# Kernel optimization log

Hardware: AMD Instinct MI355X
Metric: run time of the kernel (lower is better)

## Reference

```python
import jax, jax.numpy as jnp
import numpy as np

B, T, E, D, N, L, NF = 4, 2048, 512, 512, 16, 4, 2048


def setup_inputs() -> dict:
    key = jax.random.key(0)
    ks = jax.random.split(key, 12)
    r = lambda k, s, sc=1.0: jax.random.normal(k, s, dtype=jnp.float32) * sc
    return {
        "text_emb": r(ks[0], (B, T, E)),
        "W_in": r(ks[1], (E, D), 1.0 / np.sqrt(E).astype(np.float32)),
        "b_in": jnp.zeros((D,), jnp.float32),
        "freq_pe": r(ks[2], (NF, D), 0.02),
        # diagonal-SSM (S4D) params per layer, stacked on leading L axis
        "A_log": r(ks[3], (L, D, N), 0.5),
        "B_ssm": r(ks[4], (L, D, N), 0.5),
        "C_ssm": r(ks[5], (L, D, N), 0.5),
        "log_dt": r(ks[6], (L, D), 0.5) - 4.6,  # dt ~ 0.01
        "D_skip": r(ks[7], (L, D), 0.5),
        "ln_f0_scale": jnp.ones((D,), jnp.float32),
        "ln_f0_bias": jnp.zeros((D,), jnp.float32),
        "W_f0": r(ks[8], (D, 1), 1.0 / np.sqrt(D).astype(np.float32)),
        "b_f0": jnp.zeros((1,), jnp.float32),
        "ln_en_scale": jnp.ones((D,), jnp.float32),
        "ln_en_bias": jnp.zeros((D,), jnp.float32),
        "W_en": r(ks[9], (D, 1), 1.0 / np.sqrt(D).astype(np.float32)),
        "b_en": jnp.zeros((1,), jnp.float32),
    }


def _layernorm(x, scale, bias, eps=1e-5):
    mu = jnp.mean(x, axis=-1, keepdims=True)
    var = jnp.mean(jnp.square(x - mu), axis=-1, keepdims=True)
    return (x - mu) * jax.lax.rsqrt(var + eps) * scale + bias


def _s4_layer(h, A_log, Bm, Cm, log_dt, Dsk):
    # h: [B, T, D]; diagonal SSM with ZOH discretization, scanned over T.
    dt = jnp.exp(log_dt)                 # [D]
    A = -jnp.exp(A_log)                  # [D, N], stable (negative real)
    Abar = jnp.exp(dt[:, None] * A)      # [D, N]
    Bbar = (Abar - 1.0) / A * Bm         # [D, N]
    u_t = jnp.transpose(h, (1, 0, 2))    # [T, B, D]
    x0 = jnp.zeros((h.shape[0], h.shape[2], A.shape[1]), h.dtype)  # [B, D, N]

    def step(x, u):
        x = Abar * x + Bbar * u[..., None]          # [B, D, N]
        y = jnp.einsum('bdn,dn->bd', x, Cm)         # readout
        return x, y

    _, ys = jax.lax.scan(step, x0, u_t)             # ys: [T, B, D]
    y = jnp.transpose(ys, (1, 0, 2)) + Dsk * h      # D skip connection
    return h + jax.nn.gelu(y)                       # residual + activation


def _forward(text_emb, W_in, b_in, freq_pe, A_log, B_ssm, C_ssm, log_dt,
             D_skip, ln_f0_scale, ln_f0_bias, W_f0, b_f0,
             ln_en_scale, ln_en_bias, W_en, b_en):
    x = text_emb @ W_in + b_in                      # [B, T, D]
    Tlen = x.shape[1]
    nf = freq_pe.shape[0]
    if nf >= Tlen:                                  # static-shape crop
        freq = freq_pe[:Tlen]
    else:                                           # static-shape edge pad
        pad = jnp.repeat(freq_pe[-1:], Tlen - nf, axis=0)
        freq = jnp.concatenate([freq_pe, pad], axis=0)
    h = x + freq[None, :, :]
    for l in range(A_log.shape[0]):
        h = _s4_layer(h, A_log[l], B_ssm[l], C_ssm[l], log_dt[l], D_skip[l])
    f0 = (_layernorm(h, ln_f0_scale, ln_f0_bias) @ W_f0 + b_f0)[..., 0]
    en = (_layernorm(h, ln_en_scale, ln_en_bias) @ W_en + b_en)[..., 0]
    return f0, en


def reference(text_emb, W_in, b_in, freq_pe, A_log, B_ssm, C_ssm, log_dt,
              D_skip, ln_f0_scale, ln_f0_bias, W_f0, b_f0,
              ln_en_scale, ln_en_bias, W_en, b_en):
    return _forward(text_emb, W_in, b_in, freq_pe, A_log, B_ssm, C_ssm,
                    log_dt, D_skip, ln_f0_scale, ln_f0_bias, W_f0, b_f0,
                    ln_en_scale, ln_en_bias, W_en, b_en)
```

## Files before the change

kernel.cpp:

```cpp
#include <hip/hip_runtime.h>

#define B_   4
#define T_   2048
#define E_   512
#define D_   512
#define N_   16
#define L_   4
#define TCH  16

typedef __bf16 bf16x8 __attribute__((ext_vector_type(8)));
typedef float  f32x4  __attribute__((ext_vector_type(4)));
typedef float  f32x2  __attribute__((ext_vector_type(2)));
typedef unsigned short us8 __attribute__((ext_vector_type(8)));

__device__ __forceinline__ float us2f(unsigned short u) {
    return __uint_as_float(((unsigned int)u) << 16);
}
__device__ __forceinline__ unsigned short f2us(float f) {
    unsigned int u = __float_as_uint(f);
    unsigned int r = (u + 0x7fffu + ((u >> 16) & 1u)) >> 16;
    return (unsigned short)r;
}
__device__ __forceinline__ float ldin(const void* p, int i, unsigned int f) {
    return f ? ((const float*)p)[i] : us2f(((const unsigned short*)p)[i]);
}
__device__ __forceinline__ unsigned int probe_f32(const void* lnfs) {
    return (((const unsigned int*)lnfs)[0] == 0x3F800000u) ? 1u : 0u;
}
__device__ __forceinline__ f32x2 pk_fma(f32x2 a, f32x2 b, f32x2 c) {
    f32x2 d;
    asm("v_pk_fma_f32 %0, %1, %2, %3" : "=v"(d) : "v"(a), "v"(b), "v"(c));
    return d;
}
__device__ __forceinline__ f32x2 pk_mul(f32x2 a, f32x2 b) {
    f32x2 d;
    asm("v_pk_mul_f32 %0, %1, %2" : "=v"(d) : "v"(a), "v"(b));
    return d;
}
template<int CTRL, int RM>
__device__ __forceinline__ f32x2 dpp2(f32x2 v) {
    f32x2 r;
    r[0] = __int_as_float(__builtin_amdgcn_update_dpp(0, __float_as_int(v[0]), CTRL, RM, 0xF, true));
    r[1] = __int_as_float(__builtin_amdgcn_update_dpp(0, __float_as_int(v[1]), CTRL, RM, 0xF, true));
    return r;
}

#define PA    0
#define PB    32768
#define PC    65536
#define PDT   98304
#define PDSK  100352
#define PLFS  102400
#define PLFB  102912
#define PWF   103424
#define PLES  103936
#define PLEB  104448
#define PWEN  104960
#define PSC   105472
#define PRM_N 105474

#define NB_TEXT 2048
#define NB_PRM  413
#define NB_WT   64
#define NB_S4P  128

__global__ __launch_bounds__(256) void prep_kernel(
    const void* X, const void* Win,
    const void* A_log, const void* B_ssm, const void* C_ssm,
    const void* log_dt, const void* D_skip,
    const void* lnfs, const void* lnfb, const void* Wf0,
    const void* lnes, const void* lneb, const void* Wen,
    const void* bf0, const void* ben,
    unsigned short* __restrict__ textc, unsigned short* __restrict__ Wt,
    float* __restrict__ P, float* __restrict__ P2, float* __restrict__ P3) {
    __shared__ float tile[64 * 65];
    unsigned int f = probe_f32(lnfs);
    int bid = blockIdx.x;
    if (bid < NB_TEXT) {
        int i = (bid * 256 + threadIdx.x) * 8;
        if (f) {
            const float* xf = (const float*)X;
            us8 r;
#pragma unroll
            for (int j = 0; j < 8; j++) r[j] = f2us(xf[i + j]);
            *(us8*)(textc + i) = r;
        } else {
            *(us8*)(textc + i) = *(const us8*)((const unsigned short*)X + i);
        }
    } else if (bid < NB_TEXT + NB_PRM) {
        int i = (bid - NB_TEXT) * 256 + threadIdx.x;
        if      (i < PB)     P[i] = ldin(A_log,  i - PA,   f);
        else if (i < PC)     P[i] = ldin(B_ssm,  i - PB,   f);
        else if (i < PDT)    P[i] = ldin(C_ssm,  i - PC,   f);
        else if (i < PDSK)   P[i] = ldin(log_dt, i - PDT,  f);
        else if (i < PLFS)   P[i] = ldin(D_skip, i - PDSK, f);
        else if (i < PLFB)   P[i] = ldin(lnfs,   i - PLFS, f);
        else if (i < PWF)    P[i] = ldin(lnfb,   i - PLFB, f);
        else if (i < PLES)   P[i] = ldin(Wf0,    i - PWF,  f);
        else if (i < PLEB)   P[i] = ldin(lnes,   i - PLES, f);
        else if (i < PWEN)   P[i] = ldin(lneb,   i - PLEB, f);
        else if (i < PSC)    P[i] = ldin(Wen,    i - PWEN, f);
        else if (i == PSC)     P[i] = ldin(bf0, 0, f);
        else if (i == PSC + 1) P[i] = ldin(ben, 0, f);
    } else if (bid < NB_TEXT + NB_PRM + NB_WT) {
        int tb = bid - (NB_TEXT + NB_PRM);
        int d0 = (tb >> 3) * 64, e0 = (tb & 7) * 64;
        int r = threadIdx.x >> 6, i = threadIdx.x & 63;
#pragma unroll
        for (int k = 0; k < 16; k++) {
            int e = k * 4 + r;
            tile[e * 65 + i] = ldin(Win, (e0 + e) * D_ + d0 + i, f);
        }
        __syncthreads();
#pragma unroll
        for (int k = 0; k < 16; k++) {
            int dd = k * 4 + r;
            Wt[(size_t)(d0 + dd) * E_ + e0 + i] = f2us(tile[i * 65 + dd]);
        }
    } else {
        int i = (bid - (NB_TEXT + NB_PRM + NB_WT)) * 256 + threadIdx.x;
        int n = i & 15;
        int ld = i >> 4;
        float dt = __expf(ldin(log_dt, ld, f));
        float A  = -__expf(ldin(A_log, i, f));
        float Ab = __expf(dt * A);
        float Bb = (Ab - 1.f) / A * ldin(B_ssm, i, f);
        float l2M = 23.083120654223414f * dt * A;
        float M   = exp2f(l2M);
        int base = ld * 64 + n;
        P2[base]      = Ab;
        P2[base + 16] = Bb * ldin(C_ssm, i, f);
        P2[base + 32] = M;
        P2[base + 48] = l2M;
        float pw = M;
        size_t pb = ((size_t)ld << 8) + n;
#pragma unroll
        for (int k = 0; k < 16; k++) { P3[pb + k * 16] = pw; pw *= M; }
    }
}

__global__ __launch_bounds__(256) void gemm_kernel(const unsigned short* __restrict__ X,
                                                   const unsigned short* __restrict__ Wt,
                                                   const void* __restrict__ freq,
                                                   const void* __restrict__ b_in,
                                                   const void* __restrict__ lnfs,
                                                   float* __restrict__ H) {
    __shared__ unsigned short wlds[64 * 264];
    const unsigned int fl = probe_f32(lnfs);
    const int tid = threadIdx.x;
    const int w  = tid >> 6;
    const int ln = tid & 15;
    const int q  = (tid >> 4) & 3;
    const int d0 = blockIdx.x * 64;
    const int t0 = blockIdx.y * 128;
    const int b  = blockIdx.z;

    f32x4 acc[2][4];
#pragma unroll
    for (int i = 0; i < 2; i++)
#pragma unroll
        for (int j = 0; j < 4; j++) { acc[i][j][0]=0.f; acc[i][j][1]=0.f; acc[i][j][2]=0.f; acc[i][j][3]=0.f; }

    const size_t xbase = ((size_t)b * T_ + t0) * E_;

#pragma unroll
    for (int p = 0; p < 2; ++p) {
        if (p) __syncthreads();
#pragma unroll
        for (int it = 0; it < 8; ++it) {
            int flat = it * 256 + tid;
            int d = flat >> 5;
            int e = (flat & 31) << 3;
            bf16x8 v = *(const bf16x8*)(Wt + (size_t)(d0 + d) * E_ + p * 256 + e);
            *(bf16x8*)(wlds + d * 264 + e) = v;
        }
        __syncthreads();
#pragma unroll
        for (int s = 0; s < 8; ++s) {
            const int eo = s * 32 + q * 8;
            bf16x8 bfr[4];
#pragma unroll
            for (int j = 0; j < 4; j++)
                bfr[j] = *(const bf16x8*)(wlds + (j * 16 + ln) * 264 + eo);
#pragma unroll
            for (int sub = 0; sub < 2; ++sub) {
                const int t = w * 32 + sub * 16 + ln;
                bf16x8 afr = *(const bf16x8*)(X + xbase + (size_t)t * E_ + p * 256 + eo);
#pragma unroll
                for (int j = 0; j < 4; j++)
                    acc[sub][j] = __builtin_amdgcn_mfma_f32_16x16x32_bf16(afr, bfr[j], acc[sub][j], 0, 0, 0);
            }
        }
    }
#pragma unroll
    for (int sub = 0; sub < 2; ++sub) {
#pragma unroll
        for (int j = 0; j < 4; j++) {
            int d  = d0 + j * 16 + ln;
            int tb = t0 + w * 32 + sub * 16 + q * 4;
            float bi = ldin(b_in, d, fl);
            f32x4 o;
#pragma unroll
            for (int r4 = 0; r4 < 4; r4++)
                o[r4] = acc[sub][j][r4] + ldin(freq, (tb + r4) * D_ + d, fl) + bi;
            *(f32x4*)(H + ((size_t)b * D_ + d) * T_ + tb) = o;
        }
    }
}

__global__ __launch_bounds__(128) __attribute__((amdgpu_waves_per_eu(4, 4)))
void s4_kernel(float* __restrict__ H, const float* __restrict__ P,
               const float* __restrict__ P2, const float* __restrict__ P3) {
    __shared__ float hstate[2][16];
    const int half = threadIdx.x >> 6, lane = threadIdx.x & 63;
    const int row = blockIdx.x;
    const int d = row & (D_ - 1);
    float* gp = H + (size_t)row * T_ + half * 1024 + lane * TCH;

    float u[TCH];
#pragma unroll
    for (int k = 0; k < 4; k++) {
        f32x4 v = *(const f32x4*)(gp + k * 4);
        u[k * 4] = v[0]; u[k * 4 + 1] = v[1]; u[k * 4 + 2] = v[2]; u[k * 4 + 3] = v[3];
    }

    for (int l = 0; l < L_; ++l) {
        const float* pp = P2 + (size_t)(((l << 9) + d) << 6);
        const float* pw = P3 + ((size_t)((l << 9) + d) << 8) + ((lane & 15) << 4);
        f32x2 Ab[8], w1[8];
#pragma unroll
        for (int n = 0; n < 8; n++) Ab[n] = *(const f32x2*)(pp + 2 * n);
#pragma unroll
        for (int n = 0; n < 8; n++) w1[n] = *(const f32x2*)(pw + 2 * n);
        f32x2 b[8];
#pragma unroll
        for (int n = 0; n < 8; n++) { b[n][0] = 0.f; b[n][1] = 0.f; }
#pragma unroll
        for (int j = 0; j < TCH; j++) {
            f32x2 u2; u2[0] = u[j]; u2[1] = u[j];
#pragma unroll
            for (int n = 0; n < 8; n++) b[n] = pk_fma(Ab[n], b[n], u2);
        }
        {
            f32x2 M1[8], w2[8];
#pragma unroll
            for (int n = 0; n < 8; n++) M1[n] = *(const f32x2*)(pp + 32 + 2 * n);
#pragma unroll
            for (int n = 0; n < 8; n++) b[n] = pk_fma(M1[n], dpp2<0x111, 0xF>(b[n]), b[n]);
#pragma unroll
            for (int n = 0; n < 8; n++) M1[n] = pk_mul(M1[n], M1[n]);
#pragma unroll
            for (int n = 0; n < 8; n++) b[n] = pk_fma(M1[n], dpp2<0x112, 0xF>(b[n]), b[n]);
#pragma unroll
            for (int n = 0; n < 8; n++) M1[n] = pk_mul(M1[n], M1[n]);
#pragma unroll
            for (int n = 0; n < 8; n++) b[n] = pk_fma(M1[n], dpp2<0x114, 0xF>(b[n]), b[n]);
#pragma unroll
            for (int n = 0; n < 8; n++) M1[n] = pk_mul(M1[n], M1[n]);
#pragma unroll
            for (int n = 0; n < 8; n++) b[n] = pk_fma(M1[n], dpp2<0x118, 0xF>(b[n]), b[n]);
            bool hi16 = (lane & 16) != 0;
#pragma unroll
            for (int n = 0; n < 8; n++) {
                f32x2 M16 = pk_mul(M1[n], M1[n]);
                f32x2 wm  = pk_mul(w1[n], M16);
                w2[n][0] = hi16 ? wm[0] : w1[n][0];
                w2[n][1] = hi16 ? wm[1] : w1[n][1];
            }
#pragma unroll
            for (int n = 0; n < 8; n++) b[n] = pk_fma(w1[n], dpp2<0x142, 0xA>(b[n]), b[n]);
#pragma unroll
            for (int n = 0; n < 8; n++) b[n] = pk_fma(w2[n], dpp2<0x143, 0xC>(b[n]), b[n]);
        }
        f32x2 wh[8];
        if (half) {
            float el = (float)lane;
#pragma unroll
            for (int n = 0; n < 8; n++) {
                f32x2 l2m = *(const f32x2*)(pp + 48 + 2 * n);
                wh[n][0] = exp2f(l2m[0] * el);
                wh[n][1] = exp2f(l2m[1] * el);
            }
        }
        float Dsk = P[PDSK + l * D_ + d];
        f32x2 CB[8];
#pragma unroll
        for (int n = 0; n < 8; n++) CB[n] = *(const f32x2*)(pp + 16 + 2 * n);
        if (half == 0 && lane == 63) {
#pragma unroll
            for (int n = 0; n < 8; n++) {
                hstate[l & 1][2 * n]     = b[n][0];
                hstate[l & 1][2 * n + 1] = b[n][1];
            }
        }
        f32x2 z[8];
#pragma unroll
        for (int n = 0; n < 8; n++) z[n] = dpp2<0x138, 0xF>(b[n]);
        __syncthreads();
        if (half) {
            const float* hs = hstate[l & 1];
#pragma unroll
            for (int n = 0; n < 8; n++) {
                f32x2 h0; h0[0] = hs[2 * n]; h0[1] = hs[2 * n + 1];
                z[n] = pk_fma(wh[n], h0, z[n]);
            }
        }
#pragma unroll
        for (int j = 0; j < TCH; j++) {
            float uu = u[j];
            f32x2 u2; u2[0] = uu; u2[1] = uu;
#pragma unroll
            for (int n = 0; n < 8; n++) z[n] = pk_fma(Ab[n], z[n], u2);
            f32x2 ya; ya[0] = 0.f; ya[1] = 0.f;
            f32x2 yb; yb[0] = 0.f; yb[1] = 0.f;
#pragma unroll
            for (int n = 0; n < 8; n += 2) {
                ya = pk_fma(CB[n], z[n], ya);
                yb = pk_fma(CB[n + 1], z[n + 1], yb);
            }
            f32x2 s = ya + yb;
            float y = fmaf(Dsk, uu, s[0] + s[1]);
            float t  = fmaf(0.044715f, y * y * y, y);
            float em = exp2f(-2.30220818f * t);
            float r  = __builtin_amdgcn_rcpf(1.f + em);
            u[j] = fmaf(y, r, uu);
        }
    }
#pragma unroll
    for (int k = 0; k < 4; k++) {
        f32x4 v;
        v[0] = u[k * 4]; v[1] = u[k * 4 + 1]; v[2] = u[k * 4 + 2]; v[3] = u[k * 4 + 3];
        *(f32x4*)(gp + k * 4) = v;
    }
}

__global__ __launch_bounds__(256) void final_kernel(const float* __restrict__ H,
                                                    const float* __restrict__ P,
                                                    void* __restrict__ out,
                                                    const void* __restrict__ lnfs_raw) {
    __shared__ float red[4][8][64];
    unsigned int f = probe_f32(lnfs_raw);
    int tid = threadIdx.x;
    int w = tid >> 6, tl = tid & 63;
    int tg = blockIdx.x * 64 + tl;
    int b = tg >> 11, t = tg & (T_ - 1);
    float S1=0.f,S2=0.f,Pf=0.f,Pe=0.f,Cf=0.f,Ce=0.f,Df=0.f,De=0.f;
    const float* hp = H + ((size_t)b * D_) * T_ + t;
#pragma unroll 4
    for (int i = 0; i < 128; i++) {
        int d = w * 128 + i;
        float hv = hp[(size_t)d * T_];
        float sf = P[PLFS + d], bfv = P[PLFB + d], wf = P[PWF + d];
        float se = P[PLES + d], bev = P[PLEB + d], we = P[PWEN + d];
        S1 += hv; S2 = fmaf(hv, hv, S2);
        float tf = sf * wf, te = se * we;
        Pf = fmaf(hv, tf, Pf); Pe = fmaf(hv, te, Pe);
        Cf += tf; Ce += te;
        Df = fmaf(bfv, wf, Df); De = fmaf(bev, we, De);
    }
    red[w][0][tl]=S1; red[w][1][tl]=S2; red[w][2][tl]=Pf; red[w][3][tl]=Pe;
    red[w][4][tl]=Cf; red[w][5][tl]=Ce; red[w][6][tl]=Df; red[w][7][tl]=De;
    __syncthreads();
    if (w == 0) {
        float a[8];
#pragma unroll
        for (int k = 0; k < 8; k++)
            a[k] = red[0][k][tl] + red[1][k][tl] + red[2][k][tl] + red[3][k][tl];
        float mu  = a[0] * (1.f / 512.f);
        float var = a[1] * (1.f / 512.f) - mu * mu;
        float r   = rsqrtf(var + 1e-5f);
        float f0  = r * (a[2] - mu * a[4]) + a[6] + P[PSC + 0];
        float en  = r * (a[3] - mu * a[5]) + a[7] + P[PSC + 1];
        if (f) {
            ((float*)out)[tg]           = f0;
            ((float*)out)[B_ * T_ + tg] = en;
        } else {
            ((unsigned short*)out)[tg]           = f2us(f0);
            ((unsigned short*)out)[B_ * T_ + tg] = f2us(en);
        }
    }
}

extern "C" void kernel_launch(void* const* d_in, const int* in_sizes, int n_in,
                              void* d_out, int out_size, void* d_ws, size_t ws_size,
                              hipStream_t stream) {
    (void)in_sizes; (void)n_in; (void)out_size; (void)ws_size;
    float* ws = (float*)d_ws;
    float* P     = ws;
    float* H     = ws + 105504;
    unsigned short* textc = (unsigned short*)(ws + 4299808);
    unsigned short* Wt    = (unsigned short*)(ws + 6396960);
    float* P2    = ws + 6528032;
    float* P3    = ws + 6659104;

    prep_kernel<<<dim3(NB_TEXT + NB_PRM + NB_WT + NB_S4P), dim3(256), 0, stream>>>(
        d_in[0], d_in[1], d_in[4], d_in[5], d_in[6], d_in[7], d_in[8],
        d_in[9], d_in[10], d_in[11], d_in[13], d_in[14], d_in[15],
        d_in[12], d_in[16], textc, Wt, P, P2, P3);
    gemm_kernel<<<dim3(8, 16, 4), dim3(256), 0, stream>>>(textc, Wt, d_in[3], d_in[2], d_in[9], H);
    s4_kernel<<<dim3(2048), dim3(128), 0, stream>>>(H, P, P2, P3);
    final_kernel<<<dim3(128), dim3(256), 0, stream>>>(H, P, d_out, d_in[9]);
}
```

Measured before the change: 173.4 us.

## Split S4 scan rows across four waves with shorter per-thread chunks

The S4 scan kernel now splits each sequence row across four wavefronts of 512 timesteps, with 8 timesteps per thread instead of 16. Each wave after the first combines the end states of all earlier waves, using a new precomputed 64-step decay parameter and a per-wave shared-state array. The prep kernel rescales the per-lane decay exponent and widens the P2 parameter stride to 80 so the extra constant fits, and P3 moves accordingly. This halves the serial per-thread work and doubles the threads per block, at the cost of a small serial cross-wave combine and tighter register limits from the higher occupancy target.

```diff
diff --git a/kernel.cpp b/kernel.cpp
--- a/kernel.cpp
+++ b/kernel.cpp
@@ -6,7 +6,7 @@
 #define D_   512
 #define N_   16
 #define L_   4
-#define TCH  16
+#define TCH  8
 
 typedef __bf16 bf16x8 __attribute__((ext_vector_type(8)));
 typedef float  f32x4  __attribute__((ext_vector_type(4)));
@@ -125,13 +125,14 @@
         float A  = -__expf(ldin(A_log, i, f));
         float Ab = __expf(dt * A);
         float Bb = (Ab - 1.f) / A * ldin(B_ssm, i, f);
-        float l2M = 23.083120654223414f * dt * A;
+        float l2M = 11.541560327111707f * dt * A;
         float M   = exp2f(l2M);
-        int base = ld * 64 + n;
+        int base = ld * 80 + n;
         P2[base]      = Ab;
         P2[base + 16] = Bb * ldin(C_ssm, i, f);
         P2[base + 32] = M;
         P2[base + 48] = l2M;
+        P2[base + 64] = exp2f(64.f * l2M);
         float pw = M;
         size_t pb = ((size_t)ld << 8) + n;
 #pragma unroll
@@ -208,24 +209,24 @@
     }
 }
 
-__global__ __launch_bounds__(128) __attribute__((amdgpu_waves_per_eu(4, 4)))
+__global__ __launch_bounds__(256) __attribute__((amdgpu_waves_per_eu(8, 8)))
 void s4_kernel(float* __restrict__ H, const float* __restrict__ P,
                const float* __restrict__ P2, const float* __restrict__ P3) {
-    __shared__ float hstate[2][16];
-    const int half = threadIdx.x >> 6, lane = threadIdx.x & 63;
+    __shared__ float hstate[2][3][16];
+    const int w = threadIdx.x >> 6, lane = threadIdx.x & 63;
     const int row = blockIdx.x;
     const int d = row & (D_ - 1);
-    float* gp = H + (size_t)row * T_ + half * 1024 + lane * TCH;
+    float* gp = H + (size_t)row * T_ + w * 512 + lane * TCH;
 
     float u[TCH];
 #pragma unroll
-    for (int k = 0; k < 4; k++) {
+    for (int k = 0; k < 2; k++) {
         f32x4 v = *(const f32x4*)(gp + k * 4);
         u[k * 4] = v[0]; u[k * 4 + 1] = v[1]; u[k * 4 + 2] = v[2]; u[k * 4 + 3] = v[3];
     }
 
     for (int l = 0; l < L_; ++l) {
-        const float* pp = P2 + (size_t)(((l << 9) + d) << 6);
+        const float* pp = P2 + (size_t)((l << 9) + d) * 80;
         const float* pw = P3 + ((size_t)((l << 9) + d) << 8) + ((lane & 15) << 4);
         f32x2 Ab[8], w1[8];
 #pragma unroll
@@ -272,38 +273,47 @@
 #pragma unroll
             for (int n = 0; n < 8; n++) b[n] = pk_fma(w2[n], dpp2<0x143, 0xC>(b[n]), b[n]);
         }
-        f32x2 wh[8];
-        if (half) {
+        f32x2 wl[8];
+        if (w) {
             float el = (float)lane;
 #pragma unroll
             for (int n = 0; n < 8; n++) {
                 f32x2 l2m = *(const f32x2*)(pp + 48 + 2 * n);
-                wh[n][0] = exp2f(l2m[0] * el);
-                wh[n][1] = exp2f(l2m[1] * el);
+                wl[n][0] = exp2f(l2m[0] * el);
+                wl[n][1] = exp2f(l2m[1] * el);
             }
         }
         float Dsk = P[PDSK + l * D_ + d];
         f32x2 CB[8];
 #pragma unroll
         for (int n = 0; n < 8; n++) CB[n] = *(const f32x2*)(pp + 16 + 2 * n);
-        if (half == 0 && lane == 63) {
+        if (w < 3 && lane == 63) {
 #pragma unroll
             for (int n = 0; n < 8; n++) {
-                hstate[l & 1][2 * n]     = b[n][0];
-                hstate[l & 1][2 * n + 1] = b[n][1];
+                hstate[l & 1][w][2 * n]     = b[n][0];
+                hstate[l & 1][w][2 * n + 1] = b[n][1];
             }
         }
         f32x2 z[8];
 #pragma unroll
         for (int n = 0; n < 8; n++) z[n] = dpp2<0x138, 0xF>(b[n]);
         __syncthreads();
-        if (half) {
-            const float* hs = hstate[l & 1];
-#pragma unroll
-            for (int n = 0; n < 8; n++) {
-                f32x2 h0; h0[0] = hs[2 * n]; h0[1] = hs[2 * n + 1];
-                z[n] = pk_fma(wh[n], h0, z[n]);
-            }
+        if (w) {
+            f32x2 Msg[8], E[8];
+#pragma unroll
+            for (int n = 0; n < 8; n++) Msg[n] = *(const f32x2*)(pp + 64 + 2 * n);
+#pragma unroll
+            for (int n = 0; n < 8; n++) { E[n][0] = 0.f; E[n][1] = 0.f; }
+            for (int k = 0; k < w; ++k) {
+                const float* hs = hstate[l & 1][k];
+#pragma unroll
+                for (int n = 0; n < 8; n++) {
+                    f32x2 h0; h0[0] = hs[2 * n]; h0[1] = hs[2 * n + 1];
+                    E[n] = pk_fma(Msg[n], E[n], h0);
+                }
+            }
+#pragma unroll
+            for (int n = 0; n < 8; n++) z[n] = pk_fma(wl[n], E[n], z[n]);
         }
 #pragma unroll
         for (int j = 0; j < TCH; j++) {
@@ -327,7 +337,7 @@
         }
     }
 #pragma unroll
-    for (int k = 0; k < 4; k++) {
+    for (int k = 0; k < 2; k++) {
         f32x4 v;
         v[0] = u[k * 4]; v[1] = u[k * 4 + 1]; v[2] = u[k * 4 + 2]; v[3] = u[k * 4 + 3];
         *(f32x4*)(gp + k * 4) = v;
@@ -391,13 +401,13 @@
     unsigned short* textc = (unsigned short*)(ws + 4299808);
     unsigned short* Wt    = (unsigned short*)(ws + 6396960);
     float* P2    = ws + 6528032;
-    float* P3    = ws + 6659104;
+    float* P3    = ws + 6691872;
 
     prep_kernel<<<dim3(NB_TEXT + NB_PRM + NB_WT + NB_S4P), dim3(256), 0, stream>>>(
         d_in[0], d_in[1], d_in[4], d_in[5], d_in[6], d_in[7], d_in[8],
         d_in[9], d_in[10], d_in[11], d_in[13], d_in[14], d_in[15],
         d_in[12], d_in[16], textc, Wt, P, P2, P3);
     gemm_kernel<<<dim3(8, 16, 4), dim3(256), 0, stream>>>(textc, Wt, d_in[3], d_in[2], d_in[9], H);
-    s4_kernel<<<dim3(2048), dim3(128), 0, stream>>>(H, P, P2, P3);
+    s4_kernel<<<dim3(2048), dim3(256), 0, stream>>>(H, P, P2, P3);
     final_kernel<<<dim3(128), dim3(256), 0, stream>>>(H, P, d_out, d_in[9]);
 }
```

New measurement: 349.7 us. +101.6%, slower.
